# Performance work log

Hardware: AMD Instinct MI355X
Metric: run time of the kernel (lower is better)

## Reference

```python
import jax, jax.numpy as jnp
import numpy as np

N_NODES = 200000
N_EDGES = 6400000


def _gcn_layer(x, W, b, src, dst, n):
    # PyG GCNConv: add self loops, sym-normalize, propagate src->dst, add bias.
    loop = jnp.arange(n, dtype=src.dtype)
    s = jnp.concatenate([src, loop])
    d = jnp.concatenate([dst, loop])
    deg = jax.ops.segment_sum(jnp.ones_like(s, dtype=x.dtype), d, num_segments=n)
    dinv = jnp.where(deg > 0, jax.lax.rsqrt(deg), 0.0)
    norm = dinv[s] * dinv[d]                      # [E+N]
    h = x @ W                                     # [N, F_out]
    msg = h[s] * norm[:, None]                    # gather + scale
    out = jax.ops.segment_sum(msg, d, num_segments=n)  # scatter-add
    return out + b


def setup_inputs() -> dict:
    key = jax.random.key(0)
    ks = jax.random.split(key, 4)
    x = jax.random.normal(ks[0], (N_NODES, 3), dtype=jnp.float32)
    edge_index = jax.random.randint(ks[1], (2, N_EDGES), 0, N_NODES, dtype=jnp.int64 if jax.config.read('jax_enable_x64') else jnp.int32)
    W1 = jax.random.normal(ks[2], (3, 16), dtype=jnp.float32) * (1.0 / np.sqrt(3.0))
    b1 = jnp.zeros((16,), dtype=jnp.float32)
    W2 = jax.random.normal(ks[3], (16, 3), dtype=jnp.float32) * (1.0 / np.sqrt(16.0))
    b2 = jnp.zeros((3,), dtype=jnp.float32)
    return {"x": x, "edge_index": edge_index, "W1": W1, "b1": b1, "W2": W2, "b2": b2}


def reference(x, edge_index, W1, b1, W2, b2):
    src, dst = edge_index[0], edge_index[1]
    n = x.shape[0]
    h = _gcn_layer(x, W1, b1, src, dst, n)
    h = jax.nn.relu(h)
    out = _gcn_layer(h, W2, b2, src, dst, n)
    return out
```

## Files before the change

kernel.cpp:

```cpp
#include <hip/hip_runtime.h>

#define NN 200000
#define NE 6400000
#define NB 800
#define NWA 256
#define CHUNK 25000
#define BUFCAP 44
#define CAPB 8704
#define OVF 256

#define OFF_E    0
#define OFF_C    6963200
#define OFF_RP   6964000
#define OFF_DG   7164000
#define OFF_DINV 7364000
#define OFF_XS   7564000
#define OFF_HS2  8364000

__global__ void __launch_bounds__(1024) k_scatter(const int* __restrict__ src,
                                                  const int* __restrict__ dst,
                                                  int* __restrict__ C,
                                                  int* __restrict__ E) {
    __shared__ int wbase[NB];
    __shared__ int cnt[NB];
    __shared__ int buf[NB * BUFCAP];
    __shared__ int ovf[2 * OVF];
    __shared__ int ovfn;
    int w = blockIdx.x, t = threadIdx.x;
    for (int b = t; b < NB; b += 1024) cnt[b] = 0;
    if (t == 0) ovfn = 0;
    __syncthreads();
    int lo = w * CHUNK, hi = lo + CHUNK;
    for (int i = lo + t; i < hi; i += 1024) {
        int s = src[i], d = dst[i];
        int b = d >> 8;
        int rec = s | ((d & 255) << 18);
        int pos = atomicAdd(&cnt[b], 1);
        if (pos < BUFCAP) buf[b * BUFCAP + pos] = rec;
        else {
            int o = atomicAdd(&ovfn, 1);
            ovf[2 * o] = rec;
            ovf[2 * o + 1] = (b << 16) | pos;
        }
    }
    __syncthreads();
    for (int b = t; b < NB; b += 1024)
        wbase[b] = b * CAPB + atomicAdd(&C[b], cnt[b]);
    __syncthreads();
    for (int idx = t; idx < NB * BUFCAP; idx += 1024) {
        int b = idx / BUFCAP, j = idx - b * BUFCAP;
        int c = cnt[b];
        if (j < (c < BUFCAP ? c : BUFCAP)) E[wbase[b] + j] = buf[idx];
    }
    for (int o = t; o < ovfn; o += 1024) {
        int rec = ovf[2 * o], bp = ovf[2 * o + 1];
        E[wbase[bp >> 16] + (bp & 0xFFFF)] = rec;
    }
}

__global__ void __launch_bounds__(512) k_sort(const float* __restrict__ x, int* __restrict__ E,
                       const int* __restrict__ C,
                       int* __restrict__ RP, int* __restrict__ DG,
                       float* __restrict__ dinv, float4* __restrict__ xs4) {
    __shared__ int stg[CAPB];
    __shared__ int cnt[256];
    __shared__ int pos[256];
    int b = blockIdx.x, t = threadIdx.x;
    int lo = b * CAPB;
    int n = C[b];
    if (t < 256) cnt[t] = 0;
    __syncthreads();
    for (int i = t; i < n; i += 512) {
        int r = E[lo + i];
        stg[i] = r;
        atomicAdd(&cnt[r >> 18], 1);
    }
    __syncthreads();
    if (t < 256) pos[t] = cnt[t];
    __syncthreads();
    for (int off = 1; off < 256; off <<= 1) {
        int v = 0;
        if (t < 256 && t >= off) v = pos[t - off];
        __syncthreads();
        if (t < 256) pos[t] += v;
        __syncthreads();
    }
    if (t < 256) {
        int c = cnt[t];
        int excl = pos[t] - c;
        int node = (b << 8) + t;
        if (node < NN) {
            RP[node] = lo + excl;
            DG[node] = c;
            float di = rsqrtf(1.0f + (float)c);
            dinv[node] = di;
            xs4[node] = make_float4(x[3 * node] * di, x[3 * node + 1] * di,
                                    x[3 * node + 2] * di, 0.f);
        }
        cnt[t] = excl;
    }
    __syncthreads();
    for (int i = t; i < n; i += 512) {
        int rec = stg[i];
        int l = rec >> 18;
        int slot = atomicAdd(&cnt[l], 1);
        E[lo + slot] = rec & 0x3FFFF;
    }
}

__global__ void k_gather1(const int* __restrict__ E, const int* __restrict__ RP,
                          const int* __restrict__ DG, const float* __restrict__ dinv,
                          const float4* __restrict__ xs4, const float* __restrict__ W1,
                          const float* __restrict__ b1, const float* __restrict__ W2,
                          float4* __restrict__ hs24) {
    __shared__ float sW1[48], sb1[16], sW2[48];
    __shared__ float4 sm4[16];
    int t = threadIdx.x;
    if (t < 48) sW1[t] = W1[t];
    else if (t < 64) sb1[t - 48] = b1[t - 48];
    else if (t < 112) sW2[t - 64] = W2[t - 64];
    __syncthreads();
    int seg = t >> 4, lane = t & 15;
    int n = blockIdx.x * 16 + seg;
    int rp = RP[n], dg = DG[n];
    float s0 = 0.f, s1 = 0.f, s2 = 0.f;
    for (int j = lane; j < dg; j += 16) {
        float4 m = xs4[E[rp + j]];
        s0 += m.x; s1 += m.y; s2 += m.z;
    }
#pragma unroll
    for (int msk = 1; msk < 16; msk <<= 1) {
        s0 += __shfl_xor(s0, msk, 16);
        s1 += __shfl_xor(s1, msk, 16);
        s2 += __shfl_xor(s2, msk, 16);
    }
    if (lane == 0) {
        float di = dinv[n];
        float4 self = xs4[n];
        float a0 = di * (s0 + self.x);
        float a1 = di * (s1 + self.y);
        float a2 = di * (s2 + self.z);
        float h1[16];
#pragma unroll
        for (int k = 0; k < 16; ++k) {
            float v = a0 * sW1[k] + a1 * sW1[16 + k] + a2 * sW1[32 + k] + sb1[k];
            h1[k] = v > 0.f ? v : 0.f;
        }
        float o0 = 0.f, o1 = 0.f, o2 = 0.f;
#pragma unroll
        for (int k = 0; k < 16; ++k) {
            o0 += h1[k] * sW2[3 * k + 0];
            o1 += h1[k] * sW2[3 * k + 1];
            o2 += h1[k] * sW2[3 * k + 2];
        }
        sm4[seg] = make_float4(o0 * di, o1 * di, o2 * di, 0.f);
    }
    __syncthreads();
    if (t < 64) {
        float* dstf = (float*)(hs24 + (size_t)blockIdx.x * 16);
        dstf[t] = ((const float*)sm4)[t];
    }
}

__global__ void k_gather2(const int* __restrict__ E, const int* __restrict__ RP,
                          const int* __restrict__ DG, const float* __restrict__ dinv,
                          const float4* __restrict__ hs24, const float* __restrict__ b2,
                          float* __restrict__ out) {
    __shared__ float smo[48];
    int t = threadIdx.x;
    int seg = t >> 4, lane = t & 15;
    int n = blockIdx.x * 16 + seg;
    int rp = RP[n], dg = DG[n];
    float s0 = 0.f, s1 = 0.f, s2 = 0.f;
    for (int j = lane; j < dg; j += 16) {
        float4 m = hs24[E[rp + j]];
        s0 += m.x; s1 += m.y; s2 += m.z;
    }
#pragma unroll
    for (int msk = 1; msk < 16; msk <<= 1) {
        s0 += __shfl_xor(s0, msk, 16);
        s1 += __shfl_xor(s1, msk, 16);
        s2 += __shfl_xor(s2, msk, 16);
    }
    if (lane == 0) {
        float di = dinv[n];
        float4 self = hs24[n];
        smo[seg * 3 + 0] = di * (s0 + self.x) + b2[0];
        smo[seg * 3 + 1] = di * (s1 + self.y) + b2[1];
        smo[seg * 3 + 2] = di * (s2 + self.z) + b2[2];
    }
    __syncthreads();
    if (t < 48) out[(size_t)blockIdx.x * 48 + t] = smo[t];
}

extern "C" void kernel_launch(void* const* d_in, const int* in_sizes, int n_in,
                              void* d_out, int out_size, void* d_ws, size_t ws_size,
                              hipStream_t stream) {
    const float* x  = (const float*)d_in[0];
    const int* ei   = (const int*)d_in[1];
    const float* W1 = (const float*)d_in[2];
    const float* b1 = (const float*)d_in[3];
    const float* W2 = (const float*)d_in[4];
    const float* b2 = (const float*)d_in[5];
    const int* src = ei;
    const int* dst = ei + NE;
    float* ws = (float*)d_ws;
    int* wsi = (int*)d_ws;
    float* out = (float*)d_out;

    int* E      = wsi + OFF_E;
    int* C      = wsi + OFF_C;
    int* RP     = wsi + OFF_RP;
    int* DG     = wsi + OFF_DG;
    float* dinv = ws + OFF_DINV;
    float4* xs4 = (float4*)(ws + OFF_XS);
    float4* hs24 = (float4*)(ws + OFF_HS2);

    hipMemsetAsync(C, 0, NB * sizeof(int), stream);
    k_scatter<<<NWA, 1024, 0, stream>>>(src, dst, C, E);
    k_sort<<<NB, 512, 0, stream>>>(x, E, C, RP, DG, dinv, xs4);
    k_gather1<<<NN / 16, 256, 0, stream>>>(E, RP, DG, dinv, xs4, W1, b1, W2, hs24);
    k_gather2<<<NN / 16, 256, 0, stream>>>(E, RP, DG, dinv, hs24, b2, out);
}
```

Measured before the change: 239.7 us.

## Replace per-node CSR sort with per-bucket LDS atomic accumulation in gathers

Drops the intra-bucket counting sort that built a CSR layout (RP/DG and the rewritten E). Each gather kernel now walks its 256-node bucket's unsorted edge records and accumulates messages into shared-memory float atomics indexed by local destination. This removes the scan, the staging copy and the second pass over E. In exchange it relies on LDS float atomics, which can contend on popular nodes, and floating-point summation order becomes nondeterministic.

```diff
diff --git a/kernel.cpp b/kernel.cpp
--- a/kernel.cpp
+++ b/kernel.cpp
@@ -11,8 +11,6 @@
 
 #define OFF_E    0
 #define OFF_C    6963200
-#define OFF_RP   6964000
-#define OFF_DG   7164000
 #define OFF_DINV 7364000
 #define OFF_XS   7564000
 #define OFF_HS2  8364000
@@ -58,139 +56,115 @@
     }
 }
 
-__global__ void __launch_bounds__(512) k_sort(const float* __restrict__ x, int* __restrict__ E,
-                       const int* __restrict__ C,
-                       int* __restrict__ RP, int* __restrict__ DG,
-                       float* __restrict__ dinv, float4* __restrict__ xs4) {
-    __shared__ int stg[CAPB];
+__global__ void __launch_bounds__(512) k_count(const float* __restrict__ x,
+                                               const int* __restrict__ E,
+                                               const int* __restrict__ C,
+                                               float* __restrict__ dinv,
+                                               float4* __restrict__ xs4) {
     __shared__ int cnt[256];
-    __shared__ int pos[256];
     int b = blockIdx.x, t = threadIdx.x;
-    int lo = b * CAPB;
-    int n = C[b];
     if (t < 256) cnt[t] = 0;
     __syncthreads();
-    for (int i = t; i < n; i += 512) {
-        int r = E[lo + i];
-        stg[i] = r;
-        atomicAdd(&cnt[r >> 18], 1);
-    }
+    int lo = b * CAPB, n = C[b];
+    for (int i = t; i < n; i += 512)
+        atomicAdd(&cnt[E[lo + i] >> 18], 1);
     __syncthreads();
-    if (t < 256) pos[t] = cnt[t];
-    __syncthreads();
-    for (int off = 1; off < 256; off <<= 1) {
-        int v = 0;
-        if (t < 256 && t >= off) v = pos[t - off];
-        __syncthreads();
-        if (t < 256) pos[t] += v;
-        __syncthreads();
-    }
     if (t < 256) {
-        int c = cnt[t];
-        int excl = pos[t] - c;
         int node = (b << 8) + t;
         if (node < NN) {
-            RP[node] = lo + excl;
-            DG[node] = c;
-            float di = rsqrtf(1.0f + (float)c);
+            float di = rsqrtf(1.0f + (float)cnt[t]);
             dinv[node] = di;
             xs4[node] = make_float4(x[3 * node] * di, x[3 * node + 1] * di,
                                     x[3 * node + 2] * di, 0.f);
         }
-        cnt[t] = excl;
-    }
-    __syncthreads();
-    for (int i = t; i < n; i += 512) {
-        int rec = stg[i];
-        int l = rec >> 18;
-        int slot = atomicAdd(&cnt[l], 1);
-        E[lo + slot] = rec & 0x3FFFF;
     }
 }
 
-__global__ void k_gather1(const int* __restrict__ E, const int* __restrict__ RP,
-                          const int* __restrict__ DG, const float* __restrict__ dinv,
-                          const float4* __restrict__ xs4, const float* __restrict__ W1,
-                          const float* __restrict__ b1, const float* __restrict__ W2,
-                          float4* __restrict__ hs24) {
+__global__ void __launch_bounds__(512) k_gather1b(const int* __restrict__ E,
+                                                  const int* __restrict__ C,
+                                                  const float* __restrict__ dinv,
+                                                  const float4* __restrict__ xs4,
+                                                  const float* __restrict__ W1,
+                                                  const float* __restrict__ b1,
+                                                  const float* __restrict__ W2,
+                                                  float4* __restrict__ hs24) {
+    __shared__ float acc[256 * 3];
     __shared__ float sW1[48], sb1[16], sW2[48];
-    __shared__ float4 sm4[16];
-    int t = threadIdx.x;
+    int b = blockIdx.x, t = threadIdx.x;
     if (t < 48) sW1[t] = W1[t];
     else if (t < 64) sb1[t - 48] = b1[t - 48];
     else if (t < 112) sW2[t - 64] = W2[t - 64];
+    for (int i = t; i < 768; i += 512) acc[i] = 0.f;
     __syncthreads();
-    int seg = t >> 4, lane = t & 15;
-    int n = blockIdx.x * 16 + seg;
-    int rp = RP[n], dg = DG[n];
-    float s0 = 0.f, s1 = 0.f, s2 = 0.f;
-    for (int j = lane; j < dg; j += 16) {
-        float4 m = xs4[E[rp + j]];
-        s0 += m.x; s1 += m.y; s2 += m.z;
-    }
-#pragma unroll
-    for (int msk = 1; msk < 16; msk <<= 1) {
-        s0 += __shfl_xor(s0, msk, 16);
-        s1 += __shfl_xor(s1, msk, 16);
-        s2 += __shfl_xor(s2, msk, 16);
-    }
-    if (lane == 0) {
-        float di = dinv[n];
-        float4 self = xs4[n];
-        float a0 = di * (s0 + self.x);
-        float a1 = di * (s1 + self.y);
-        float a2 = di * (s2 + self.z);
-        float h1[16];
-#pragma unroll
-        for (int k = 0; k < 16; ++k) {
-            float v = a0 * sW1[k] + a1 * sW1[16 + k] + a2 * sW1[32 + k] + sb1[k];
-            h1[k] = v > 0.f ? v : 0.f;
-        }
-        float o0 = 0.f, o1 = 0.f, o2 = 0.f;
-#pragma unroll
-        for (int k = 0; k < 16; ++k) {
-            o0 += h1[k] * sW2[3 * k + 0];
-            o1 += h1[k] * sW2[3 * k + 1];
-            o2 += h1[k] * sW2[3 * k + 2];
-        }
-        sm4[seg] = make_float4(o0 * di, o1 * di, o2 * di, 0.f);
+    int lo = b * CAPB, n = C[b];
+#pragma unroll 4
+    for (int i = t; i < n; i += 512) {
+        int rec = E[lo + i];
+        float4 m = xs4[rec & 0x3FFFF];
+        int dl = (rec >> 18) * 3;
+        atomicAdd(&acc[dl + 0], m.x);
+        atomicAdd(&acc[dl + 1], m.y);
+        atomicAdd(&acc[dl + 2], m.z);
     }
     __syncthreads();
-    if (t < 64) {
-        float* dstf = (float*)(hs24 + (size_t)blockIdx.x * 16);
-        dstf[t] = ((const float*)sm4)[t];
+    if (t < 256) {
+        int node = (b << 8) + t;
+        if (node < NN) {
+            float di = dinv[node];
+            float4 self = xs4[node];
+            float a0 = di * (acc[3 * t + 0] + self.x);
+            float a1 = di * (acc[3 * t + 1] + self.y);
+            float a2 = di * (acc[3 * t + 2] + self.z);
+            float o0 = 0.f, o1 = 0.f, o2 = 0.f;
+#pragma unroll
+            for (int k = 0; k < 16; ++k) {
+                float v = a0 * sW1[k] + a1 * sW1[16 + k] + a2 * sW1[32 + k] + sb1[k];
+                v = v > 0.f ? v : 0.f;
+                o0 += v * sW2[3 * k + 0];
+                o1 += v * sW2[3 * k + 1];
+                o2 += v * sW2[3 * k + 2];
+            }
+            hs24[node] = make_float4(o0 * di, o1 * di, o2 * di, 0.f);
+        }
     }
 }
 
-__global__ void k_gather2(const int* __restrict__ E, const int* __restrict__ RP,
-                          const int* __restrict__ DG, const float* __restrict__ dinv,
-                          const float4* __restrict__ hs24, const float* __restrict__ b2,
-                          float* __restrict__ out) {
-    __shared__ float smo[48];
-    int t = threadIdx.x;
-    int seg = t >> 4, lane = t & 15;
-    int n = blockIdx.x * 16 + seg;
-    int rp = RP[n], dg = DG[n];
-    float s0 = 0.f, s1 = 0.f, s2 = 0.f;
-    for (int j = lane; j < dg; j += 16) {
-        float4 m = hs24[E[rp + j]];
-        s0 += m.x; s1 += m.y; s2 += m.z;
-    }
-#pragma unroll
-    for (int msk = 1; msk < 16; msk <<= 1) {
-        s0 += __shfl_xor(s0, msk, 16);
-        s1 += __shfl_xor(s1, msk, 16);
-        s2 += __shfl_xor(s2, msk, 16);
-    }
-    if (lane == 0) {
-        float di = dinv[n];
-        float4 self = hs24[n];
-        smo[seg * 3 + 0] = di * (s0 + self.x) + b2[0];
-        smo[seg * 3 + 1] = di * (s1 + self.y) + b2[1];
-        smo[seg * 3 + 2] = di * (s2 + self.z) + b2[2];
+__global__ void __launch_bounds__(512) k_gather2b(const int* __restrict__ E,
+                                                  const int* __restrict__ C,
+                                                  const float* __restrict__ dinv,
+                                                  const float4* __restrict__ hs24,
+                                                  const float* __restrict__ b2,
+                                                  float* __restrict__ out) {
+    __shared__ float acc[256 * 3];
+    __shared__ float smo[256 * 3];
+    int b = blockIdx.x, t = threadIdx.x;
+    for (int i = t; i < 768; i += 512) acc[i] = 0.f;
+    __syncthreads();
+    int lo = b * CAPB, n = C[b];
+#pragma unroll 4
+    for (int i = t; i < n; i += 512) {
+        int rec = E[lo + i];
+        float4 m = hs24[rec & 0x3FFFF];
+        int dl = (rec >> 18) * 3;
+        atomicAdd(&acc[dl + 0], m.x);
+        atomicAdd(&acc[dl + 1], m.y);
+        atomicAdd(&acc[dl + 2], m.z);
     }
     __syncthreads();
-    if (t < 48) out[(size_t)blockIdx.x * 48 + t] = smo[t];
+    if (t < 256) {
+        int node = (b << 8) + t;
+        if (node < NN) {
+            float di = dinv[node];
+            float4 self = hs24[node];
+            smo[3 * t + 0] = di * (acc[3 * t + 0] + self.x) + b2[0];
+            smo[3 * t + 1] = di * (acc[3 * t + 1] + self.y) + b2[1];
+            smo[3 * t + 2] = di * (acc[3 * t + 2] + self.z) + b2[2];
+        }
+    }
+    __syncthreads();
+    int base = (b << 8) * 3;
+    for (int i = t; i < 768; i += 512)
+        if (base + i < NN * 3) out[base + i] = smo[i];
 }
 
 extern "C" void kernel_launch(void* const* d_in, const int* in_sizes, int n_in,
@@ -210,15 +184,13 @@
 
     int* E      = wsi + OFF_E;
     int* C      = wsi + OFF_C;
-    int* RP     = wsi + OFF_RP;
-    int* DG     = wsi + OFF_DG;
     float* dinv = ws + OFF_DINV;
     float4* xs4 = (float4*)(ws + OFF_XS);
     float4* hs24 = (float4*)(ws + OFF_HS2);
 
     hipMemsetAsync(C, 0, NB * sizeof(int), stream);
     k_scatter<<<NWA, 1024, 0, stream>>>(src, dst, C, E);
-    k_sort<<<NB, 512, 0, stream>>>(x, E, C, RP, DG, dinv, xs4);
-    k_gather1<<<NN / 16, 256, 0, stream>>>(E, RP, DG, dinv, xs4, W1, b1, W2, hs24);
-    k_gather2<<<NN / 16, 256, 0, stream>>>(E, RP, DG, dinv, hs24, b2, out);
+    k_count<<<NB, 512, 0, stream>>>(x, E, C, dinv, xs4);
+    k_gather1b<<<NB, 512, 0, stream>>>(E, C, dinv, xs4, W1, b1, W2, hs24);
+    k_gather2b<<<NB, 512, 0, stream>>>(E, C, dinv, hs24, b2, out);
 }
```

After: 385.3 us. +60.7%, slower.
